# Performance work log

Hardware: AMD Instinct MI355X
Metric: run time of the kernel (lower is better)

Reference implementation:

```python
import jax, jax.numpy as jnp
import numpy as np
import math

B, N, DIM = 2, 2048, 1024
D_LAYERS, H, DH = 6, 8, 64
INNER = H * DH            # 512
FF_IN = int(DIM * 2 * 4 / 3)  # 2730 (GEGLU inner dim)
NB, MD = 32, 128          # rel-pos buckets / max distance
ALPHA = 0.1               # grad_shrink alpha
EPS = 1e-5


def setup_inputs() -> dict:
    key = jax.random.key(0)
    ks = jax.random.split(key, 8)
    s = 0.02
    return {
        "x": jax.random.normal(ks[0], (B, N, DIM), jnp.float32),
        "rel_emb": jax.random.normal(ks[1], (NB, H), jnp.float32) * s,
        "ln1_g": jnp.ones((D_LAYERS, DIM), jnp.float32),
        "ln1_b": jnp.zeros((D_LAYERS, DIM), jnp.float32),
        "wq": jax.random.normal(ks[2], (D_LAYERS, DIM, INNER), jnp.float32) * s,
        "wkv": jax.random.normal(ks[3], (D_LAYERS, DIM, 2 * DH), jnp.float32) * s,
        "wo": jax.random.normal(ks[4], (D_LAYERS, INNER, DIM), jnp.float32) * s,
        "ln2_g": jnp.ones((D_LAYERS, DIM), jnp.float32),
        "ln2_b": jnp.zeros((D_LAYERS, DIM), jnp.float32),
        "w1": jax.random.normal(ks[5], (D_LAYERS, DIM, 2 * FF_IN), jnp.float32) * s,
        "w2": jax.random.normal(ks[6], (D_LAYERS, FF_IN, DIM), jnp.float32) * s,
        "lnf_g": jnp.ones((DIM,), jnp.float32),
        "lnf_b": jnp.zeros((DIM,), jnp.float32),
    }


def _ln(x, g, b):
    mu = jnp.mean(x, axis=-1, keepdims=True)
    var = jnp.mean(jnp.square(x - mu), axis=-1, keepdims=True)
    return (x - mu) * jax.lax.rsqrt(var + EPS) * g + b


def _rel_pos_bias(rel_emb, n):
    pos = jnp.arange(n)
    rel = pos[None, :] - pos[:, None]        # k_pos - q_pos
    dist = jnp.maximum(-rel, 0)
    max_exact = NB // 2
    is_small = dist < max_exact
    val_large = max_exact + (
        jnp.log(jnp.maximum(dist, 1).astype(jnp.float32) / max_exact)
        / math.log(MD / max_exact) * (NB - max_exact)
    ).astype(jnp.int32)
    val_large = jnp.minimum(val_large, NB - 1)
    bucket = jnp.where(is_small, dist, val_large)
    return jnp.transpose(rel_emb[bucket], (2, 0, 1))  # [H, n, n]


def reference(x, rel_emb, ln1_g, ln1_b, wq, wkv, wo, ln2_g, ln2_b, w1, w2, lnf_g, lnf_b):
    b, n, _ = x.shape
    scale = DH ** -0.5
    # grad_shrink (forward identity, scales gradient by alpha)
    x = x * ALPHA + jax.lax.stop_gradient(x) * (1.0 - ALPHA)
    bias = _rel_pos_bias(rel_emb, n)               # [H, n, n]
    causal = jnp.triu(jnp.ones((n, n), bool), 1)   # mask above diagonal
    neg = -jnp.finfo(x.dtype).max
    for l in range(D_LAYERS):
        # --- causal self-attention (multi-query: shared k/v) ---
        xn = _ln(x, ln1_g[l], ln1_b[l])
        q = (xn @ wq[l]).reshape(b, n, H, DH).transpose(0, 2, 1, 3) * scale  # bhnd
        k, v = jnp.split(xn @ wkv[l], 2, axis=-1)                            # [b,n,DH] each
        sim = jnp.einsum('bhid,bjd->bhij', q, k) + bias[None]
        sim = jnp.where(causal, neg, sim)
        attn = jax.nn.softmax(sim, axis=-1)
        o = jnp.einsum('bhij,bjd->bhid', attn, v).transpose(0, 2, 1, 3).reshape(b, n, INNER)
        x = x + o @ wo[l]
        # --- GEGLU feedforward ---
        xn = _ln(x, ln2_g[l], ln2_b[l])
        h = xn @ w1[l]
        a, g = jnp.split(h, 2, axis=-1)
        x = x + (jax.nn.gelu(g, approximate=False) * a) @ w2[l]
    return _ln(x, lnf_g, lnf_b)
```

## Files before the change

kernel.cpp:

```cpp
#include <hip/hip_runtime.h>
#include <cstdint>
#include <cstddef>

using bf16 = __bf16;
typedef __bf16 bf16x8 __attribute__((ext_vector_type(8)));
typedef __bf16 bf16x4 __attribute__((ext_vector_type(4)));
typedef __bf16 bf16x2 __attribute__((ext_vector_type(2)));
typedef float  f32x4  __attribute__((ext_vector_type(4)));
typedef float  f32x16 __attribute__((ext_vector_type(16)));
typedef int    i32x4  __attribute__((ext_vector_type(4)));
typedef float  f32x4u __attribute__((ext_vector_type(4), aligned(4)));

constexpr int NB   = 2;
constexpr int NN   = 2048;
constexpr int DIM  = 1024;
constexpr int NH   = 8;
constexpr int DH   = 64;
constexpr int INNER= 512;
constexpr int QKVN = 640;
constexpr int FF   = 2730;
constexpr int FFP  = 2816;
constexpr int FF2N = 5632;
constexpr int MROW = NB * NN;
constexpr int NLAY = 6;
constexpr int AROWS = NB * NH * NN;
constexpr int NSPLIT = 4;

__device__ __forceinline__ void gload_lds16(const bf16* g, bf16* l) {
  __builtin_amdgcn_global_load_lds((const __attribute__((address_space(1))) void*)g,
                                   (__attribute__((address_space(3))) void*)l,
                                   16, 0, 0);
}

__device__ __forceinline__ int pack_bf16(float lo, float hi_) {
  bf16x2 t; t[0] = (bf16)lo; t[1] = (bf16)hi_;
  return __builtin_bit_cast(int, t);
}

__global__ void btab_kernel(const float* __restrict__ rel, float* __restrict__ btab) {
  int d = blockIdx.x * 256 + threadIdx.x;
  if (d >= NN) return;
  int bucket;
  if (d < 16) bucket = d;
  else {
    int vl = 16 + (int)(logf((float)d / 16.0f) / logf(8.0f) * 16.0f);
    bucket = vl < 31 ? vl : 31;
  }
  for (int h = 0; h < NH; ++h) btab[h * NN + d] = rel[bucket * NH + h];
}

__global__ void conv_tr(const float* __restrict__ src, size_t srcLayer, int srcStride,
                        int colOff, int R, int C,
                        bf16* __restrict__ dst, size_t dstLayer, int Tcols, float scale,
                        int rowOff16) {
  __shared__ float tile[32][33];
  const int i0 = blockIdx.x * 32, j0 = blockIdx.y * 32, z = blockIdx.z;
  const float* s = src + (size_t)z * srcLayer;
  bf16* d = dst + (size_t)z * dstLayer;
  const int tx = threadIdx.x, ty = threadIdx.y;
#pragma unroll
  for (int k = 0; k < 4; ++k) {
    int j = j0 + ty + k * 8;
    int i = i0 + tx;
    float v = 0.0f;
    if (j < R && i < C) v = s[(size_t)j * srcStride + colOff + i] * scale;
    tile[ty + k * 8][tx] = v;
  }
  __syncthreads();
#pragma unroll
  for (int k = 0; k < 4; ++k) {
    int i = i0 + ty + k * 8;
    int j = j0 + tx;
    int dr = (rowOff16 >= 0) ? (((i >> 4) << 5) + rowOff16 + (i & 15)) : i;
    d[(size_t)dr * Tcols + j] = (bf16)tile[tx][ty + k * 8];
  }
}

template <typename OUT>
__global__ void ln_kernel(const float* __restrict__ X, const float* __restrict__ G,
                          const float* __restrict__ Bt, OUT* __restrict__ out) {
  __shared__ float red[8];
  const int row = blockIdx.x, t = threadIdx.x;
  const float* xr = X + (size_t)row * DIM;
  float4 v = *(const float4*)(xr + t * 4);
  float s  = v.x + v.y + v.z + v.w;
  float s2 = v.x * v.x + v.y * v.y + v.z * v.z + v.w * v.w;
#pragma unroll
  for (int o = 1; o < 64; o <<= 1) { s += __shfl_xor(s, o); s2 += __shfl_xor(s2, o); }
  if ((t & 63) == 0) { red[t >> 6] = s; red[4 + (t >> 6)] = s2; }
  __syncthreads();
  float S  = red[0] + red[1] + red[2] + red[3];
  float S2 = red[4] + red[5] + red[6] + red[7];
  const float inv = 1.0f / (float)DIM;
  float mu = S * inv;
  float var = S2 * inv - mu * mu;
  float rstd = rsqrtf(var + 1e-5f);
  float4 g  = *(const float4*)(G + t * 4);
  float4 bb = *(const float4*)(Bt + t * 4);
  OUT* orow = out + (size_t)row * DIM + t * 4;
  orow[0] = (OUT)((v.x - mu) * rstd * g.x + bb.x);
  orow[1] = (OUT)((v.y - mu) * rstd * g.y + bb.y);
  orow[2] = (OUT)((v.z - mu) * rstd * g.z + bb.z);
  orow[3] = (OUT)((v.w - mu) * rstd * g.w + bb.w);
}

template <int MODE>
__launch_bounds__(512)
__global__ void gemm_bt(const bf16* __restrict__ A, const bf16* __restrict__ B,
                        int K, int lda, int N, bf16* __restrict__ Cb, float* __restrict__ Xr) {
  __shared__ __align__(16) bf16 As[2][128 * 64];
  __shared__ __align__(16) bf16 Bs[2][128 * 64];
  const int tid = threadIdx.x;
  const int lane = tid & 63, wave = tid >> 6;
  const int gx = gridDim.x, gy = gridDim.y;
  const int nwg = gx * gy;
  const int orig = blockIdx.y * gx + blockIdx.x;
  const int wgid = (orig & 7) * (nwg >> 3) + (orig >> 3);
  const int m0 = (wgid % gy) * 128;
  const int n0 = (wgid / gy) * 128;
  const int wm = (wave >> 2) * 64, wn = (wave & 3) * 32;
  const int fr = lane & 15, fg8 = (lane >> 4) * 8;
  const int frl8 = (fr & 7) * 8;
  const int rL = lane >> 3;
  const int cS = ((lane & 7) ^ rL) * 8;
  const bf16* aB = A + (size_t)(m0 + wave * 8 + rL) * lda + cS;
  const bf16* bB = B + (size_t)(n0 + wave * 8 + rL) * K + cS;
  f32x4 acc[4][2] = {};

  auto STAGE = [&](int buf, int kt) {
#pragma unroll
    for (int r = 0; r < 2; ++r) {
      gload_lds16(aB + (size_t)(r * 64) * lda + kt, &As[buf][(r * 8 + wave) * 512]);
      gload_lds16(bB + (size_t)(r * 64) * K + kt, &Bs[buf][(r * 8 + wave) * 512]);
    }
  };

  STAGE(0, 0);
  const int nt = K >> 6;
  int cur = 0;
  for (int t = 0; t < nt; ++t) {
    asm volatile("s_waitcnt vmcnt(0)" ::: "memory");
    __builtin_amdgcn_s_barrier();
    __builtin_amdgcn_sched_barrier(0);
    if (t + 1 < nt) STAGE(cur ^ 1, (t + 1) * 64);
#pragma unroll
    for (int kk = 0; kk < 64; kk += 32) {
      bf16x8 af[4], bfr[2];
#pragma unroll
      for (int m = 0; m < 4; ++m)
        af[m] = *(const bf16x8*)&As[cur][(wm + m * 16 + fr) * 64 + ((kk + fg8) ^ frl8)];
#pragma unroll
      for (int n = 0; n < 2; ++n)
        bfr[n] = *(const bf16x8*)&Bs[cur][(wn + n * 16 + fr) * 64 + ((kk + fg8) ^ frl8)];
#pragma unroll
      for (int m = 0; m < 4; ++m)
#pragma unroll
        for (int n = 0; n < 2; ++n)
          acc[m][n] = __builtin_amdgcn_mfma_f32_16x16x32_bf16(af[m], bfr[n], acc[m][n], 0, 0, 0);
    }
    __builtin_amdgcn_sched_barrier(0);
    __builtin_amdgcn_s_barrier();
    cur ^= 1;
  }
  const int cc = lane & 15, cg = (lane >> 4) * 4;
  if (MODE == 2) {
    const int jcol = (n0 + wn) / 2 + cc;
#pragma unroll
    for (int m = 0; m < 4; ++m) {
#pragma unroll
      for (int r = 0; r < 4; ++r) {
        const int row = m0 + wm + m * 16 + cg + r;
        const float av = acc[m][0][r], gv = acc[m][1][r];
        const float ge = 0.5f * gv * (1.0f + erff(gv * 0.70710678118654752f)) * av;
        Cb[(size_t)row * N + jcol] = (bf16)ge;
      }
    }
  } else {
#pragma unroll
    for (int m = 0; m < 4; ++m) {
#pragma unroll
      for (int n = 0; n < 2; ++n) {
        const int col = n0 + wn + n * 16 + cc;
#pragma unroll
        for (int r = 0; r < 4; ++r) {
          const int row = m0 + wm + m * 16 + cg + r;
          const size_t idx = (size_t)row * N + col;
          if (MODE == 0) Cb[idx] = (bf16)acc[m][n][r];
          else           Xr[idx] += acc[m][n][r];
        }
      }
    }
  }
}

__global__ void vt_kernel(const bf16* __restrict__ QKV, bf16* __restrict__ VT) {
  __shared__ bf16 t[32][33];
  const int n0 = blockIdx.x * 32, d0 = blockIdx.y * 32, b = blockIdx.z;
  const int tx = threadIdx.x, ty = threadIdx.y;
#pragma unroll
  for (int k = 0; k < 4; ++k) {
    int n = n0 + ty + k * 8;
    t[ty + k * 8][tx] = QKV[(size_t)(b * NN + n) * QKVN + 576 + d0 + tx];
  }
  __syncthreads();
#pragma unroll
  for (int k = 0; k < 4; ++k) {
    int dh = d0 + ty + k * 8;
    VT[(size_t)(b * 64 + dh) * NN + n0 + tx] = t[tx][ty + k * 8];
  }
}

__launch_bounds__(256)
__global__ void attn_kernel(const bf16* __restrict__ QKV, const bf16* __restrict__ VT,
                            const float* __restrict__ btab,
                            float* __restrict__ Opart, float* __restrict__ mlbuf) {
  const int tid = threadIdx.x;
  const int lane = tid & 63, wv = tid >> 6;
  const int split = blockIdx.x & (NSPLIT - 1);
  const int qt = (NN / 32 - 1) - (blockIdx.x / NSPLIT);
  const int h = blockIdx.y * 4 + wv, b = blockIdx.z;
  const int q0 = qt * 32;
  const int qc = lane & 31;
  const int hid = lane >> 5;
  const int h8 = hid * 8;
  const int kv_full = q0 + 32;
  const int nt32 = kv_full >> 5;
  const int base = nt32 >> 2, rem = nt32 & 3;
  const int cnt = base + (split < rem ? 1 : 0);
  const int startT = split * base + (split < rem ? split : rem);
  const int lo = startT * 32;
  const int kend = lo + cnt * 32;
  const size_t obase = ((size_t)(split * NB * NH) + b * NH + h) * NN;
  const int Rbase = (b * NH + h) * NN + q0;
  float* prow = Opart + (obase + q0 + qc) * 64;
  if (cnt == 0) {
#pragma unroll
    for (int dd = 0; dd < 32; ++dd) prow[dd * 2 + hid] = 0.0f;
    if (hid == 0)
      ((float2*)mlbuf)[(size_t)split * AROWS + Rbase + qc] = make_float2(-1e30f, 0.0f);
    return;
  }
  const float* bt = btab + h * NN;
  bf16x8 qf[4];
#pragma unroll
  for (int ks = 0; ks < 4; ++ks)
    qf[ks] = *(const bf16x8*)&QKV[(size_t)(b * NN + q0 + qc) * QKVN + h * DH + ks * 16 + h8];

  f32x16 Oacc0 = {}, Oacc1 = {};
  float m_run = -1e30f, l_run = 0.0f;
  int kv0 = lo;

  while (kv0 < kend) {
    const bool interior = (kv0 + 32 <= q0);
    bf16x8 kf[4];
#pragma unroll
    for (int ks = 0; ks < 4; ++ks)
      kf[ks] = *(const bf16x8*)&QKV[(size_t)(b * NN + kv0 + qc) * QKVN + 512 + ks * 16 + h8];
    bf16x8 vf[2][2];
#pragma unroll
    for (int dblk = 0; dblk < 2; ++dblk)
#pragma unroll
      for (int ks2 = 0; ks2 < 2; ++ks2)
        vf[dblk][ks2] = *(const bf16x8*)&VT[(size_t)(b * 64 + dblk * 32 + qc) * NN + kv0 + ks2 * 16 + h8];
    __builtin_amdgcn_s_setprio(1);
    f32x16 S = {};
#pragma unroll
    for (int ks = 0; ks < 4; ++ks)
      S = __builtin_amdgcn_mfma_f32_32x32x16_bf16(kf[ks], qf[ks], S, 0, 0, 0);
    __builtin_amdgcn_s_setprio(0);
    float sv[16];
    float mx = -1e30f;
    if (interior) {
      f32x4 bv[4];
#pragma unroll
      for (int g = 0; g < 4; ++g)
        bv[g] = *(const f32x4u*)(bt + (q0 + qc - kv0 - 8 * g - 4 * hid - 3));
#pragma unroll
      for (int g = 0; g < 4; ++g)
#pragma unroll
        for (int e = 0; e < 4; ++e) {
          const float val = S[g * 4 + e] + bv[g][3 - e];
          sv[g * 4 + e] = val;
          mx = fmaxf(mx, val);
        }
    } else {
#pragma unroll
      for (int r = 0; r < 16; ++r) {
        const int kvr = (r & 3) + 8 * (r >> 2) + 4 * hid;
        const int d = (q0 + qc) - (kv0 + kvr);
        const int dc = d > 0 ? d : 0;
        float val = S[r] + bt[dc];
        if (d < 0) val = -1e30f;
        sv[r] = val;
        mx = fmaxf(mx, val);
      }
    }
    if (!__all(mx <= m_run + 8.0f)) {
      mx = fmaxf(mx, __shfl_xor(mx, 32));
      const float m_new = fmaxf(m_run, mx);
      const float sc = __expf(m_run - m_new);
      l_run *= sc;
#pragma unroll
      for (int r = 0; r < 16; ++r) { Oacc0[r] *= sc; Oacc1[r] *= sc; }
      m_run = m_new;
    }
    float csum = 0.0f;
#pragma unroll
    for (int r = 0; r < 16; ++r) { sv[r] = __expf(sv[r] - m_run); csum += sv[r]; }
    csum += __shfl_xor(csum, 32);
    l_run += csum;
    int w[8];
#pragma unroll
    for (int g = 0; g < 4; ++g) {
      w[2 * g]     = pack_bf16(sv[4 * g],     sv[4 * g + 1]);
      w[2 * g + 1] = pack_bf16(sv[4 * g + 2], sv[4 * g + 3]);
    }
    bf16x8 pfrag[2];
#pragma unroll
    for (int ks2 = 0; ks2 < 2; ++ks2) {
      const int a  = w[4 * ks2],     bb = w[4 * ks2 + 1];
      const int c  = w[4 * ks2 + 2], dd = w[4 * ks2 + 3];
      const int s0 = hid ? a : c,    s1 = hid ? bb : dd;
      const int r0 = __shfl_xor(s0, 32);
      const int r1 = __shfl_xor(s1, 32);
      i32x4 fw;
      fw[0] = hid ? r0 : a;
      fw[1] = hid ? r1 : bb;
      fw[2] = hid ? c  : r0;
      fw[3] = hid ? dd : r1;
      pfrag[ks2] = __builtin_bit_cast(bf16x8, fw);
    }
    __builtin_amdgcn_s_setprio(1);
#pragma unroll
    for (int ks2 = 0; ks2 < 2; ++ks2) {
      Oacc0 = __builtin_amdgcn_mfma_f32_32x32x16_bf16(vf[0][ks2], pfrag[ks2], Oacc0, 0, 0, 0);
      Oacc1 = __builtin_amdgcn_mfma_f32_32x32x16_bf16(vf[1][ks2], pfrag[ks2], Oacc1, 0, 0, 0);
    }
    __builtin_amdgcn_s_setprio(0);
    kv0 += 32;
  }
#pragma unroll
  for (int r = 0; r < 16; ++r) {
    const int dl = (r & 3) + 8 * (r >> 2) + 4 * hid;
    prow[dl]      = Oacc0[r];
    prow[32 + dl] = Oacc1[r];
  }
  if (hid == 0)
    ((float2*)mlbuf)[(size_t)split * AROWS + Rbase + qc] = make_float2(m_run, l_run);
}

__global__ void attn_combine(const float* __restrict__ Opart, const float* __restrict__ mlbuf,
                             bf16* __restrict__ O) {
  const int gtid = blockIdx.x * 256 + threadIdx.x;
  const int dq = gtid & 15;
  const int q  = (gtid >> 4) & (NN - 1);
  const int bh = gtid >> 15;
  const int R = bh * NN + q;
  float2 ml[NSPLIT];
  float m = -1e30f;
#pragma unroll
  for (int s = 0; s < NSPLIT; ++s) {
    ml[s] = ((const float2*)mlbuf)[(size_t)s * AROWS + R];
    m = fmaxf(m, ml[s].x);
  }
  float w[NSPLIT];
  float denom = 0.0f;
#pragma unroll
  for (int s = 0; s < NSPLIT; ++s) {
    w[s] = __expf(ml[s].x - m);
    denom += ml[s].y * w[s];
  }
  const float inv = 1.0f / denom;
  float o[4] = {};
#pragma unroll
  for (int s = 0; s < NSPLIT; ++s) {
    const f32x4 v = *(const f32x4*)(Opart + ((size_t)(s * NB * NH + bh) * NN + q) * 64 + dq * 4);
#pragma unroll
    for (int j = 0; j < 4; ++j) o[j] += v[j] * w[s];
  }
  bf16x4 res;
#pragma unroll
  for (int j = 0; j < 4; ++j) res[j] = (bf16)(o[j] * inv);
  const int h = bh & (NH - 1), b = bh >> 3;
  *(bf16x4*)&O[(size_t)(b * NN + q) * INNER + h * DH + dq * 4] = res;
}

extern "C" void kernel_launch(void* const* d_in, const int* in_sizes, int n_in,
                              void* d_out, int out_size, void* d_ws, size_t ws_size,
                              hipStream_t stream) {
  (void)in_sizes; (void)n_in; (void)out_size;
  const float* in_x  = (const float*)d_in[0];
  const float* rel   = (const float*)d_in[1];
  const float* ln1g  = (const float*)d_in[2];
  const float* ln1b  = (const float*)d_in[3];
  const float* wq    = (const float*)d_in[4];
  const float* wkv   = (const float*)d_in[5];
  const float* wo    = (const float*)d_in[6];
  const float* ln2g  = (const float*)d_in[7];
  const float* ln2b  = (const float*)d_in[8];
  const float* w1    = (const float*)d_in[9];
  const float* w2    = (const float*)d_in[10];
  const float* lnfg  = (const float*)d_in[11];
  const float* lnfb  = (const float*)d_in[12];
  float* out = (float*)d_out;

  constexpr size_t E_QKV = (size_t)QKVN * DIM;
  constexpr size_t E_WO  = (size_t)DIM * INNER;
  constexpr size_t E_W1F = (size_t)FF2N * DIM;
  constexpr size_t E_W2  = (size_t)DIM * FFP;
  bf16* wqkvT = (bf16*)d_ws;
  bf16* woT  = wqkvT + NLAY * E_QKV;
  bf16* w1fT = woT  + NLAY * E_WO;
  bf16* w2T  = w1fT + NLAY * E_W1F;
  bf16* xnb  = w2T  + NLAY * E_W2;
  bf16* qkvb = xnb  + (size_t)MROW * DIM;
  bf16* vTb  = qkvb + (size_t)MROW * QKVN;
  bf16* ob   = vTb  + (size_t)NB * 64 * NN;
  bf16* hb   = ob   + (size_t)MROW * INNER;
  float* xbuf = (float*)(hb + (size_t)MROW * FF2N);
  float* btab = xbuf + (size_t)MROW * DIM;
  const size_t needed = (size_t)((char*)(btab + NH * NN) - (char*)d_ws);
  if (ws_size < needed) return;
  float* Opart = (float*)hb;
  float* mlbuf = (float*)(hb + (size_t)18 * 1024 * 1024);
  hipMemcpyAsync(xbuf, in_x, (size_t)MROW * DIM * sizeof(float),
                 hipMemcpyDeviceToDevice, stream);
  btab_kernel<<<8, 256, 0, stream>>>(rel, btab);

  const dim3 tb(32, 8);
  conv_tr<<<dim3(16, 32, 6), tb, 0, stream>>>(wq,  (size_t)DIM*INNER, INNER, 0, DIM, INNER,
                                              wqkvT, E_QKV, DIM, 0.125f, -1);
  conv_tr<<<dim3(4, 32, 6),  tb, 0, stream>>>(wkv, (size_t)DIM*128, 128, 0, DIM, 128,
                                              wqkvT + (size_t)INNER*DIM, E_QKV, DIM, 1.0f, -1);
  conv_tr<<<dim3(32, 16, 6), tb, 0, stream>>>(wo,  (size_t)INNER*DIM, DIM, 0, INNER, DIM,
                                              woT,  E_WO, INNER, 1.0f, -1);
  conv_tr<<<dim3(88, 32, 6), tb, 0, stream>>>(w1,  (size_t)DIM*2*FF, 2*FF, 0, DIM, FF,
                                              w1fT, E_W1F, DIM, 1.0f, 0);
  conv_tr<<<dim3(88, 32, 6), tb, 0, stream>>>(w1,  (size_t)DIM*2*FF, 2*FF, FF, DIM, FF,
                                              w1fT, E_W1F, DIM, 1.0f, 16);
  conv_tr<<<dim3(32, 88, 6), tb, 0, stream>>>(w2,  (size_t)FF*DIM, DIM, 0, FF, DIM,
                                              w2T,  E_W2, FFP, 1.0f, -1);

  for (int l = 0; l < NLAY; ++l) {
    ln_kernel<bf16><<<MROW, 256, 0, stream>>>(xbuf, ln1g + l*DIM, ln1b + l*DIM, xnb);
    gemm_bt<0><<<dim3(QKVN/128, MROW/128), 512, 0, stream>>>(xnb, wqkvT + l*E_QKV, DIM, DIM, QKVN, qkvb, nullptr);
    vt_kernel<<<dim3(NN/32, 2, NB), tb, 0, stream>>>(qkvb, vTb);
    attn_kernel<<<dim3((NN/32)*NSPLIT, NH/4, NB), 256, 0, stream>>>(qkvb, vTb, btab, Opart, mlbuf);
    attn_combine<<<AROWS*16/256, 256, 0, stream>>>(Opart, mlbuf, ob);
    gemm_bt<1><<<dim3(DIM/128, MROW/128), 512, 0, stream>>>(ob, woT + l*E_WO, INNER, INNER, DIM, nullptr, xbuf);
    ln_kernel<bf16><<<MROW, 256, 0, stream>>>(xbuf, ln2g + l*DIM, ln2b + l*DIM, xnb);
    gemm_bt<2><<<dim3(FF2N/128, MROW/128), 512, 0, stream>>>(xnb, w1fT + l*E_W1F, DIM, DIM, FFP, hb, nullptr);
    gemm_bt<1><<<dim3(DIM/128, MROW/128), 512, 0, stream>>>(hb, w2T + l*E_W2, FFP, FFP, DIM, nullptr, xbuf);
  }
  ln_kernel<float><<<MROW, 256, 0, stream>>>(xbuf, lnfg, lnfb, out);
}
```

Before: 1.668 ms.

## Use dedicated 256-thread single-buffered GEMM with XCD remap for GEGLU up-projection

Adds a new gemm97 kernel for the W1/GEGLU projection. It uses 4 waves, each computing a 64x64 sub-tile (4x4 MFMA fragments), single-buffered LDS, and a workgroup-id remap that groups tiles per XCD. The GEGLU epilogue pairs adjacent fragments. The generic gemm_bt loses its MODE 2 path. Larger per-wave tiles raise register reuse, but the lack of double buffering may expose load latency.

```diff
diff --git a/kernel.cpp b/kernel.cpp
--- a/kernel.cpp
+++ b/kernel.cpp
@@ -163,23 +163,90 @@
     cur ^= 1;
   }
   const int cc = lane & 15, cg = (lane >> 4) * 4;
-  if (MODE == 2) {
-    const int jcol = (n0 + wn) / 2 + cc;
-#pragma unroll
-    for (int m = 0; m < 4; ++m) {
+#pragma unroll
+  for (int m = 0; m < 4; ++m) {
+#pragma unroll
+    for (int n = 0; n < 2; ++n) {
+      const int col = n0 + wn + n * 16 + cc;
 #pragma unroll
       for (int r = 0; r < 4; ++r) {
         const int row = m0 + wm + m * 16 + cg + r;
-        const float av = acc[m][0][r], gv = acc[m][1][r];
-        const float ge = 0.5f * gv * (1.0f + erff(gv * 0.70710678118654752f)) * av;
-        Cb[(size_t)row * N + jcol] = (bf16)ge;
+        const size_t idx = (size_t)row * N + col;
+        if (MODE == 0) Cb[idx] = (bf16)acc[m][n][r];
+        else           Xr[idx] += acc[m][n][r];
       }
     }
+  }
+}
+
+template <int MODE>
+__launch_bounds__(256)
+__global__ void gemm97(const bf16* __restrict__ A, const bf16* __restrict__ B,
+                       int K, int lda, int N, bf16* __restrict__ Cb, float* __restrict__ Xr) {
+  __shared__ __align__(16) bf16 As[128 * 64];
+  __shared__ __align__(16) bf16 Bs[128 * 64];
+  const int tid = threadIdx.x;
+  const int lane = tid & 63, wave = tid >> 6;
+  const int gx = gridDim.x, gy = gridDim.y;
+  const int nwg = gx * gy;
+  const int orig = blockIdx.y * gx + blockIdx.x;
+  const int wgid = (orig & 7) * (nwg >> 3) + (orig >> 3);
+  const int m0 = (wgid % gy) * 128;
+  const int n0 = (wgid / gy) * 128;
+  const int wm = (wave >> 1) * 64, wn = (wave & 1) * 64;
+  const int fr = lane & 15, fg8 = (lane >> 4) * 8;
+  const int frl8 = (fr & 7) * 8;
+  const int rL = lane >> 3;
+  const int cS = ((lane & 7) ^ rL) * 8;
+  const bf16* aB = A + (size_t)(m0 + wave * 8 + rL) * lda + cS;
+  const bf16* bB = B + (size_t)(n0 + wave * 8 + rL) * K + cS;
+  f32x4 acc[4][4] = {};
+
+  for (int kt = 0; kt < K; kt += 64) {
+    __syncthreads();
+#pragma unroll
+    for (int r = 0; r < 4; ++r) {
+      gload_lds16(aB + (size_t)(r * 32) * lda + kt, &As[(r * 4 + wave) * 512]);
+      gload_lds16(bB + (size_t)(r * 32) * K + kt, &Bs[(r * 4 + wave) * 512]);
+    }
+    __syncthreads();
+#pragma unroll
+    for (int kk = 0; kk < 64; kk += 32) {
+      bf16x8 af[4], bfr[4];
+#pragma unroll
+      for (int m = 0; m < 4; ++m)
+        af[m] = *(const bf16x8*)&As[(wm + m * 16 + fr) * 64 + ((kk + fg8) ^ frl8)];
+#pragma unroll
+      for (int n = 0; n < 4; ++n)
+        bfr[n] = *(const bf16x8*)&Bs[(wn + n * 16 + fr) * 64 + ((kk + fg8) ^ frl8)];
+#pragma unroll
+      for (int m = 0; m < 4; ++m)
+#pragma unroll
+        for (int n = 0; n < 4; ++n)
+          acc[m][n] = __builtin_amdgcn_mfma_f32_16x16x32_bf16(af[m], bfr[n], acc[m][n], 0, 0, 0);
+    }
+  }
+  const int cc = lane & 15, cg = (lane >> 4) * 4;
+  if (MODE == 2) {
+    const int jbase = (n0 + wn) / 2 + cc;
+#pragma unroll
+    for (int m = 0; m < 4; ++m) {
+#pragma unroll
+      for (int p = 0; p < 2; ++p) {
+#pragma unroll
+        for (int r = 0; r < 4; ++r) {
+          const int row = m0 + wm + m * 16 + cg + r;
+          const float av = acc[m][2 * p][r], gv = acc[m][2 * p + 1][r];
+          const float ge = 0.5f * gv * (1.0f + erff(gv * 0.70710678118654752f)) * av;
+          Cb[(size_t)row * N + jbase + p * 16] = (bf16)ge;
+        }
+      }
+    }
   } else {
 #pragma unroll
     for (int m = 0; m < 4; ++m) {
 #pragma unroll
-      for (int n = 0; n < 2; ++n) {
+      for (int n = 0; n < 4; ++n) {
         const int col = n0 + wn + n * 16 + cc;
 #pragma unroll
         for (int r = 0; r < 4; ++r) {
@@ -449,7 +516,7 @@
     attn_combine<<<AROWS*16/256, 256, 0, stream>>>(Opart, mlbuf, ob);
     gemm_bt<1><<<dim3(DIM/128, MROW/128), 512, 0, stream>>>(ob, woT + l*E_WO, INNER, INNER, DIM, nullptr, xbuf);
     ln_kernel<bf16><<<MROW, 256, 0, stream>>>(xbuf, ln2g + l*DIM, ln2b + l*DIM, xnb);
-    gemm_bt<2><<<dim3(FF2N/128, MROW/128), 512, 0, stream>>>(xnb, w1fT + l*E_W1F, DIM, DIM, FFP, hb, nullptr);
+    gemm97<2><<<dim3(FF2N/128, MROW/128), 256, 0, stream>>>(xnb, w1fT + l*E_W1F, DIM, DIM, FFP, hb, nullptr);
     gemm_bt<1><<<dim3(DIM/128, MROW/128), 512, 0, stream>>>(hb, w2T + l*E_W2, FFP, FFP, DIM, nullptr, xbuf);
   }
   ln_kernel<float><<<MROW, 256, 0, stream>>>(xbuf, lnfg, lnfb, out);
```

Measured after the change: 1.604 ms. -3.8%, faster.
